# Performance work log

Hardware: AMD Instinct MI355X
Metric: run time of the kernel (lower is better)

## Reference

```python
import jax, jax.numpy as jnp
import numpy as np

B, C, H, W = 16, 512, 32, 32
G = min(C // 4, 32)  # group-norm groups = 32
EPS = 1e-6


def setup_inputs() -> dict:
    key = jax.random.key(0)
    ks = jax.random.split(key, 9)
    s = 1.0 / np.sqrt(C)
    return {
        "x": jax.random.normal(ks[0], (B, C, H, W), dtype=jnp.float32),
        "gn_gamma": jnp.ones((C,), jnp.float32),
        "gn_beta": jnp.zeros((C,), jnp.float32),
        "W0": jax.random.normal(ks[1], (C, C), jnp.float32) * s,
        "b0": jnp.zeros((C,), jnp.float32),
        "W1": jax.random.normal(ks[2], (C, C), jnp.float32) * s,
        "b1": jnp.zeros((C,), jnp.float32),
        "W2": jax.random.normal(ks[3], (C, C), jnp.float32) * s,
        "b2": jnp.zeros((C,), jnp.float32),
        "W3": jax.random.normal(ks[4], (C, C), jnp.float32) * s,
        "b3": jnp.zeros((C,), jnp.float32),
    }


def _group_norm(x, gamma, beta):
    b, c, h, w = x.shape
    xg = x.reshape(b, G, c // G, h, w)
    mu = jnp.mean(xg, axis=(2, 3, 4), keepdims=True)
    var = jnp.var(xg, axis=(2, 3, 4), keepdims=True)
    xn = ((xg - mu) * jax.lax.rsqrt(var + EPS)).reshape(b, c, h, w)
    return xn * gamma[None, :, None, None] + beta[None, :, None, None]


def _nin(x, Wm, bv):
    # 1x1 conv via channel contraction: bchw,cd->bdhw
    return jnp.einsum('bchw,cd->bdhw', x, Wm) + bv[None, :, None, None]


def reference(x, gn_gamma, gn_beta, W0, b0, W1, b1, W2, b2, W3, b3):
    b, c, h, w = x.shape
    hn = _group_norm(x, gn_gamma, gn_beta)
    q = _nin(hn, W0, b0)
    k = _nin(hn, W1, b1)
    v = _nin(hn, W2, b2)
    # attention scores over all spatial positions: [b, h, w, i, j]
    scores = jnp.einsum('bchw,bcij->bhwij', q, k) * (c ** -0.5)
    attn = jax.nn.softmax(scores.reshape(b, h, w, h * w), axis=-1).reshape(b, h, w, h, w)
    o = jnp.einsum('bhwij,bcij->bchw', attn, v)
    o = _nin(o, W3, b3)
    return x + o  # skip_rescale=False
```

## Files before the change

### kernel.cpp

```cpp
#include <hip/hip_runtime.h>
#include <stdint.h>

typedef __bf16 bf16_t;
typedef _Float16 f16_t;
typedef bf16_t bf16x8 __attribute__((ext_vector_type(8)));
typedef bf16_t bf16x4 __attribute__((ext_vector_type(4)));
typedef f16_t  f16x8  __attribute__((ext_vector_type(8)));
typedef float floatx4 __attribute__((ext_vector_type(4)));

static constexpr int NB  = 16;
static constexpr int NC  = 512;
static constexpr int NHW = 1024;
static constexpr int NG  = 32;
static constexpr int CPG = 16;

#define SCALE 0.044194173824159216f
#define LOG2E 1.4426950408889634f

__global__ __launch_bounds__(256) void gn_stats_k(const float* __restrict__ x,
                                                  float* __restrict__ stats) {
  int bg = blockIdx.x;
  const float* xp = x + (size_t)bg * CPG * NHW;
  float s = 0.f, ss = 0.f;
  for (int i = threadIdx.x * 4; i < CPG * NHW; i += 256 * 4) {
    float4 v = *(const float4*)&xp[i];
    s += v.x + v.y + v.z + v.w;
    ss += v.x * v.x + v.y * v.y + v.z * v.z + v.w * v.w;
  }
#pragma unroll
  for (int off = 1; off < 64; off <<= 1) {
    s  += __shfl_xor(s,  off, 64);
    ss += __shfl_xor(ss, off, 64);
  }
  __shared__ float red[2][4];
  int wv = threadIdx.x >> 6;
  if ((threadIdx.x & 63) == 0) { red[0][wv] = s; red[1][wv] = ss; }
  __syncthreads();
  if (threadIdx.x == 0) {
    float st  = red[0][0] + red[0][1] + red[0][2] + red[0][3];
    float sst = red[1][0] + red[1][1] + red[1][2] + red[1][3];
    float mean = st * (1.f / 16384.f);
    float var  = sst * (1.f / 16384.f) - mean * mean;
    stats[bg * 2]     = mean;
    stats[bg * 2 + 1] = rsqrtf(var + 1e-6f);
  }
}

__global__ __launch_bounds__(256) void gn_apply_k(const float* __restrict__ x,
                                                  const float* __restrict__ gamma,
                                                  const float* __restrict__ beta,
                                                  const float* __restrict__ stats,
                                                  bf16_t* __restrict__ hnT) {
  int bi = blockIdx.z;
  int c0 = blockIdx.y * 32;
  int n0 = blockIdx.x * 32;
  __shared__ float tile[32][33];
  int tn = threadIdx.x & 31;
  int tr = threadIdx.x >> 5;
  const float* xb = x + (size_t)bi * NC * NHW;
#pragma unroll
  for (int r = 0; r < 4; r++) {
    int c = c0 + tr + r * 8;
    int g = c >> 4;
    float mean = stats[(bi * NG + g) * 2];
    float rstd = stats[(bi * NG + g) * 2 + 1];
    float ga = gamma[c], be = beta[c];
    float v = xb[(size_t)c * NHW + n0 + tn];
    tile[tr + r * 8][tn] = (v - mean) * rstd * ga + be;
  }
  __syncthreads();
  bf16_t* hb = hnT + (size_t)bi * NHW * NC;
#pragma unroll
  for (int r = 0; r < 4; r++)
    hb[(size_t)(n0 + tr + r * 8) * NC + c0 + tn] = (bf16_t)tile[tn][tr + r * 8];
}

__global__ __launch_bounds__(256) void wtrans_k(const float* __restrict__ W0,
                                                const float* __restrict__ W1,
                                                const float* __restrict__ W2,
                                                const float* __restrict__ W3,
                                                bf16_t* __restrict__ Wt) {
  int w = blockIdx.z;
  const float* W = (w == 0) ? W0 : (w == 1) ? W1 : (w == 2) ? W2 : W3;
  int d0 = blockIdx.x * 32, c0 = blockIdx.y * 32;
  __shared__ float tile[32][33];
  int tdx = threadIdx.x & 31, tr = threadIdx.x >> 5;
#pragma unroll
  for (int r = 0; r < 4; r++)
    tile[tr + r * 8][tdx] = W[(size_t)(c0 + tr + r * 8) * NC + d0 + tdx];
  __syncthreads();
  bf16_t* o = Wt + (size_t)w * NC * NC;
#pragma unroll
  for (int r = 0; r < 4; r++)
    o[(size_t)(d0 + tr + r * 8) * NC + c0 + tdx] = (bf16_t)tile[tdx][tr + r * 8];
}

__device__ __forceinline__ void glds16(const bf16_t* g, bf16_t* lds) {
  __builtin_amdgcn_global_load_lds(
      (const __attribute__((address_space(1))) unsigned int*)g,
      (__attribute__((address_space(3))) unsigned int*)lds, 16, 0, 0);
}

template<int KDIM>
__device__ __forceinline__ void gemm_core128(const bf16_t* __restrict__ A,
                                             const bf16_t* __restrict__ B,
                                             int m0, int n0,
                                             floatx4 (&acc)[4][4]) {
  __shared__ bf16_t As[128 * 32];
  __shared__ bf16_t Bs[128 * 32];
  const int tid = threadIdx.x, lane = tid & 63, wv = tid >> 6;
  const int l16 = lane & 15, quad = lane >> 4;
  const int wm = wv & 1, wn = wv >> 1;

  const bf16_t* aptr = A + (size_t)(m0 + wv * 32 + (lane >> 2)) * KDIM + (lane & 3) * 8;
  const bf16_t* bptr = B + (size_t)(n0 + wv * 32 + (lane >> 2)) * KDIM + (lane & 3) * 8;
  bf16_t* as0 = &As[(wv * 32) * 32];
  bf16_t* as1 = &As[(wv * 32 + 16) * 32];
  bf16_t* bs0 = &Bs[(wv * 32) * 32];
  bf16_t* bs1 = &Bs[(wv * 32 + 16) * 32];

  for (int k0 = 0; k0 < KDIM; k0 += 32) {
    __syncthreads();
    glds16(aptr, as0);
    glds16(aptr + (size_t)16 * KDIM, as1);
    glds16(bptr, bs0);
    glds16(bptr + (size_t)16 * KDIM, bs1);
    aptr += 32; bptr += 32;
    __syncthreads();
    bf16x8 af[4], bfv[4];
#pragma unroll
    for (int i = 0; i < 4; i++)
      af[i] = *(const bf16x8*)&As[(wm * 64 + i * 16 + l16) * 32 + quad * 8];
#pragma unroll
    for (int j = 0; j < 4; j++)
      bfv[j] = *(const bf16x8*)&Bs[(wn * 64 + j * 16 + l16) * 32 + quad * 8];
#pragma unroll
    for (int i = 0; i < 4; i++)
#pragma unroll
      for (int j = 0; j < 4; j++)
        acc[i][j] = __builtin_amdgcn_mfma_f32_16x16x32_bf16(af[i], bfv[j], acc[i][j], 0, 0, 0);
  }
}

__global__ __launch_bounds__(256) void gemm_qkv2_k(const bf16_t* __restrict__ hnT,
                                                   const bf16_t* __restrict__ Wt,
                                                   const float* __restrict__ b0,
                                                   const float* __restrict__ b1,
                                                   const float* __restrict__ b2,
                                                   bf16_t* __restrict__ Qt,
                                                   bf16_t* __restrict__ Kt,
                                                   bf16_t* __restrict__ Vm) {
  int bz = blockIdx.z, bi = bz & 15, wsel = bz >> 4;
  int n0 = blockIdx.x * 128, m0 = blockIdx.y * 128;
  const bf16_t* A = hnT + (size_t)bi * NHW * NC;
  const bf16_t* B = Wt + (size_t)wsel * NC * NC;
  floatx4 acc[4][4];
#pragma unroll
  for (int i = 0; i < 4; i++)
#pragma unroll
    for (int j = 0; j < 4; j++) acc[i][j] = (floatx4){0.f, 0.f, 0.f, 0.f};
  gemm_core128<NC>(A, B, m0, n0, acc);

  const int lane = threadIdx.x & 63, wv = threadIdx.x >> 6;
  const int l16 = lane & 15, quad = lane >> 4, wm = wv & 1, wn = wv >> 1;
  const float* bias = (wsel == 0) ? b0 : (wsel == 1) ? b1 : b2;
  if (wsel < 2) {
    bf16_t* out = ((wsel == 0) ? Qt : Kt) + (size_t)bi * NHW * NC;
#pragma unroll
    for (int i = 0; i < 4; i++)
#pragma unroll
      for (int j = 0; j < 4; j++) {
        int row = m0 + wm * 64 + i * 16 + quad * 4;
        int col = n0 + wn * 64 + j * 16 + l16;
        float bv = bias[col];
#pragma unroll
        for (int r = 0; r < 4; r++)
          out[(size_t)(row + r) * NC + col] = (bf16_t)(acc[i][j][r] + bv);
      }
  } else {
    bf16_t* out = Vm + (size_t)bi * NC * NHW;
#pragma unroll
    for (int i = 0; i < 4; i++)
#pragma unroll
      for (int j = 0; j < 4; j++) {
        int row = m0 + wm * 64 + i * 16 + quad * 4;
        int col = n0 + wn * 64 + j * 16 + l16;
        float bv = bias[col];
        bf16x4 pk;
#pragma unroll
        for (int r = 0; r < 4; r++) pk[r] = (bf16_t)(acc[i][j][r] + bv);
        *(bf16x4*)&out[(size_t)col * NHW + row] = pk;
      }
  }
}

__global__ __launch_bounds__(256) void gemm_s_k(const bf16_t* __restrict__ Qt,
                                                const bf16_t* __restrict__ Kt,
                                                f16_t* __restrict__ S) {
  int bi = blockIdx.z;
  int n0 = blockIdx.x * 128, m0 = blockIdx.y * 128;
  const bf16_t* A = Qt + (size_t)bi * NHW * NC;
  const bf16_t* B = Kt + (size_t)bi * NHW * NC;
  floatx4 acc[4][4];
#pragma unroll
  for (int i = 0; i < 4; i++)
#pragma unroll
    for (int j = 0; j < 4; j++) acc[i][j] = (floatx4){0.f, 0.f, 0.f, 0.f};
  gemm_core128<NC>(A, B, m0, n0, acc);

  const int lane = threadIdx.x & 63, wv = threadIdx.x >> 6;
  const int l16 = lane & 15, quad = lane >> 4, wm = wv & 1, wn = wv >> 1;
  f16_t* out = S + (size_t)bi * NHW * NHW;
#pragma unroll
  for (int i = 0; i < 4; i++)
#pragma unroll
    for (int j = 0; j < 4; j++) {
      int row = m0 + wm * 64 + i * 16 + quad * 4;
      int col = n0 + wn * 64 + j * 16 + l16;
#pragma unroll
      for (int r = 0; r < 4; r++)
        out[(size_t)(row + r) * NHW + col] = (f16_t)(acc[i][j][r] * SCALE);
    }
}

__global__ __launch_bounds__(256) void softmax_k(const f16_t* __restrict__ S,
                                                 bf16_t* __restrict__ P) {
  int row = blockIdx.x * 4 + (threadIdx.x >> 6);
  int lane = threadIdx.x & 63;
  const f16_t* sp = S + (size_t)row * NHW + lane * 16;
  f16x8 a = *(const f16x8*)sp;
  f16x8 b = *(const f16x8*)(sp + 8);
  float v[16];
#pragma unroll
  for (int k = 0; k < 8; k++) { v[k] = (float)a[k]; v[8 + k] = (float)b[k]; }
  float mx = v[0];
#pragma unroll
  for (int k = 1; k < 16; k++) mx = fmaxf(mx, v[k]);
#pragma unroll
  for (int off = 1; off < 64; off <<= 1) mx = fmaxf(mx, __shfl_xor(mx, off, 64));
  float e[16], s = 0.f;
#pragma unroll
  for (int k = 0; k < 16; k++) { e[k] = exp2f((v[k] - mx) * LOG2E); s += e[k]; }
#pragma unroll
  for (int off = 1; off < 64; off <<= 1) s += __shfl_xor(s, off, 64);
  float inv = 1.f / s;
  bf16x8 o0, o1;
#pragma unroll
  for (int k = 0; k < 8; k++) { o0[k] = (bf16_t)(e[k] * inv); o1[k] = (bf16_t)(e[8 + k] * inv); }
  bf16_t* pp = P + (size_t)row * NHW + lane * 16;
  *(bf16x8*)pp = o0;
  *(bf16x8*)(pp + 8) = o1;
}

__global__ __launch_bounds__(256) void gemm_pv_k(const bf16_t* __restrict__ P,
                                                 const bf16_t* __restrict__ Vm,
                                                 bf16_t* __restrict__ Ot) {
  int bi = blockIdx.z;
  int n0 = blockIdx.x * 128, m0 = blockIdx.y * 128;
  const bf16_t* A = P + (size_t)bi * NHW * NHW;
  const bf16_t* B = Vm + (size_t)bi * NC * NHW;
  floatx4 acc[4][4];
#pragma unroll
  for (int i = 0; i < 4; i++)
#pragma unroll
    for (int j = 0; j < 4; j++) acc[i][j] = (floatx4){0.f, 0.f, 0.f, 0.f};
  gemm_core128<NHW>(A, B, m0, n0, acc);

  const int lane = threadIdx.x & 63, wv = threadIdx.x >> 6;
  const int l16 = lane & 15, quad = lane >> 4, wm = wv & 1, wn = wv >> 1;
  bf16_t* out = Ot + (size_t)bi * NHW * NC;
#pragma unroll
  for (int i = 0; i < 4; i++)
#pragma unroll
    for (int j = 0; j < 4; j++) {
      int row = m0 + wm * 64 + i * 16 + quad * 4;
      int col = n0 + wn * 64 + j * 16 + l16;
#pragma unroll
      for (int r = 0; r < 4; r++)
        out[(size_t)(row + r) * NC + col] = (bf16_t)(acc[i][j][r]);
    }
}

__global__ __launch_bounds__(256) void gemm_fin_k(const bf16_t* __restrict__ Ot,
                                                  const bf16_t* __restrict__ W3t,
                                                  const float* __restrict__ b3,
                                                  const float* __restrict__ x,
                                                  float* __restrict__ outp) {
  int bi = blockIdx.z;
  int n0 = blockIdx.x * 128, m0 = blockIdx.y * 128;
  const bf16_t* A = Ot + (size_t)bi * NHW * NC;
  floatx4 acc[4][4];
#pragma unroll
  for (int i = 0; i < 4; i++)
#pragma unroll
    for (int j = 0; j < 4; j++) acc[i][j] = (floatx4){0.f, 0.f, 0.f, 0.f};
  gemm_core128<NC>(A, W3t, m0, n0, acc);

  const int lane = threadIdx.x & 63, wv = threadIdx.x >> 6;
  const int l16 = lane & 15, quad = lane >> 4, wm = wv & 1, wn = wv >> 1;
  const float* xb = x + (size_t)bi * NC * NHW;
  float* ob = outp + (size_t)bi * NC * NHW;
#pragma unroll
  for (int i = 0; i < 4; i++)
#pragma unroll
    for (int j = 0; j < 4; j++) {
      int row = m0 + wm * 64 + i * 16 + quad * 4;
      int col = n0 + wn * 64 + j * 16 + l16;
      float bv = b3[col];
      size_t base = (size_t)col * NHW + row;
      float4 xv = *(const float4*)&xb[base];
      float4 pk;
      pk.x = acc[i][j][0] + bv + xv.x;
      pk.y = acc[i][j][1] + bv + xv.y;
      pk.z = acc[i][j][2] + bv + xv.z;
      pk.w = acc[i][j][3] + bv + xv.w;
      *(float4*)&ob[base] = pk;
    }
}

extern "C" void kernel_launch(void* const* d_in, const int* in_sizes, int n_in,
                              void* d_out, int out_size, void* d_ws, size_t ws_size,
                              hipStream_t stream) {
  (void)in_sizes; (void)n_in; (void)out_size; (void)ws_size;
  const float* x     = (const float*)d_in[0];
  const float* gamma = (const float*)d_in[1];
  const float* beta  = (const float*)d_in[2];
  const float* W0    = (const float*)d_in[3];
  const float* b0    = (const float*)d_in[4];
  const float* W1    = (const float*)d_in[5];
  const float* b1    = (const float*)d_in[6];
  const float* W2    = (const float*)d_in[7];
  const float* b2    = (const float*)d_in[8];
  const float* W3    = (const float*)d_in[9];
  const float* b3    = (const float*)d_in[10];
  float* outp = (float*)d_out;

  char* ws = (char*)d_ws;
  const size_t PLANE = (size_t)NB * NHW * NC * sizeof(bf16_t);
  float* stats = (float*)ws;
  size_t off = 4096;
  bf16_t* hnT = (bf16_t*)(ws + off); off += PLANE;
  bf16_t* Qt  = (bf16_t*)(ws + off); off += PLANE;
  bf16_t* Kt  = (bf16_t*)(ws + off); off += PLANE;
  bf16_t* Vm  = (bf16_t*)(ws + off); off += PLANE;
  bf16_t* Wt  = (bf16_t*)(ws + off); off += 4 * (size_t)NC * NC * sizeof(bf16_t);
  f16_t*  S   = (f16_t*)(ws + off);  off += (size_t)NB * NHW * NHW * sizeof(f16_t);
  bf16_t* P   = (bf16_t*)S;
  bf16_t* Ot  = hnT;

  gn_stats_k<<<NB * NG, 256, 0, stream>>>(x, stats);
  gn_apply_k<<<dim3(32, 16, NB), 256, 0, stream>>>(x, gamma, beta, stats, hnT);
  wtrans_k<<<dim3(16, 16, 4), 256, 0, stream>>>(W0, W1, W2, W3, Wt);
  gemm_qkv2_k<<<dim3(4, 8, 48), 256, 0, stream>>>(hnT, Wt, b0, b1, b2, Qt, Kt, Vm);
  gemm_s_k<<<dim3(8, 8, NB), 256, 0, stream>>>(Qt, Kt, S);
  softmax_k<<<dim3(NB * NHW / 4), 256, 0, stream>>>(S, P);
  gemm_pv_k<<<dim3(4, 8, NB), 256, 0, stream>>>(P, Vm, Ot);
  gemm_fin_k<<<dim3(4, 8, NB), 256, 0, stream>>>(Ot, Wt + 3 * (size_t)NC * NC, b3, x, outp);
}
```

Before: 259.6 us.

## Widen GEMM K-tile to 64 with XOR-swizzled LDS and vectorized epilogue stores

The shared GEMM core now stages 64-wide K tiles, with an XOR swizzle on the LDS chunk index to avoid bank conflicts. This halves the number of barrier pairs per K loop. A SWAP template option exchanges the MFMA operands so that row-major outputs (Q/K, S, PV) can be written as packed 4-element vector stores instead of scattered scalar stores. The QKV GEMM is split into separate Q/K and V kernels, and the transpose kernels now write packed bf16x4. The cost is double the LDS per block, which may lower occupancy.

```diff
diff --git a/kernel.cpp b/kernel.cpp
--- a/kernel.cpp
+++ b/kernel.cpp
@@ -6,6 +6,7 @@
 typedef bf16_t bf16x8 __attribute__((ext_vector_type(8)));
 typedef bf16_t bf16x4 __attribute__((ext_vector_type(4)));
 typedef f16_t  f16x8  __attribute__((ext_vector_type(8)));
+typedef f16_t  f16x4  __attribute__((ext_vector_type(4)));
 typedef float floatx4 __attribute__((ext_vector_type(4)));
 
 static constexpr int NB  = 16;
@@ -70,9 +71,11 @@
   }
   __syncthreads();
   bf16_t* hb = hnT + (size_t)bi * NHW * NC;
-#pragma unroll
-  for (int r = 0; r < 4; r++)
-    hb[(size_t)(n0 + tr + r * 8) * NC + c0 + tn] = (bf16_t)tile[tn][tr + r * 8];
+  int nl = threadIdx.x >> 3, cc = (threadIdx.x & 7) * 4;
+  bf16x4 pk;
+#pragma unroll
+  for (int i = 0; i < 4; i++) pk[i] = (bf16_t)tile[cc + i][nl];
+  *(bf16x4*)&hb[(size_t)(n0 + nl) * NC + c0 + cc] = pk;
 }
 
 __global__ __launch_bounds__(256) void wtrans_k(const float* __restrict__ W0,
@@ -90,9 +93,11 @@
     tile[tr + r * 8][tdx] = W[(size_t)(c0 + tr + r * 8) * NC + d0 + tdx];
   __syncthreads();
   bf16_t* o = Wt + (size_t)w * NC * NC;
-#pragma unroll
-  for (int r = 0; r < 4; r++)
-    o[(size_t)(d0 + tr + r * 8) * NC + c0 + tdx] = (bf16_t)tile[tdx][tr + r * 8];
+  int dl = threadIdx.x >> 3, cc = (threadIdx.x & 7) * 4;
+  bf16x4 pk;
+#pragma unroll
+  for (int i = 0; i < 4; i++) pk[i] = (bf16_t)tile[cc + i][dl];
+  *(bf16x4*)&o[(size_t)(d0 + dl) * NC + c0 + cc] = pk;
 }
 
 __device__ __forceinline__ void glds16(const bf16_t* g, bf16_t* lds) {
@@ -101,97 +106,123 @@
       (__attribute__((address_space(3))) unsigned int*)lds, 16, 0, 0);
 }
 
-template<int KDIM>
-__device__ __forceinline__ void gemm_core128(const bf16_t* __restrict__ A,
-                                             const bf16_t* __restrict__ B,
-                                             int m0, int n0,
-                                             floatx4 (&acc)[4][4]) {
-  __shared__ bf16_t As[128 * 32];
-  __shared__ bf16_t Bs[128 * 32];
+__device__ __forceinline__ floatx4 mfma_bf16(bf16x8 a, bf16x8 b, floatx4 c) {
+  return __builtin_amdgcn_mfma_f32_16x16x32_bf16(a, b, c, 0, 0, 0);
+}
+
+template<int KDIM, bool SWAP>
+__device__ __forceinline__ void gemm_core(const bf16_t* __restrict__ A,
+                                          const bf16_t* __restrict__ B,
+                                          int m0, int n0,
+                                          floatx4 (&acc)[4][4]) {
+  __shared__ bf16_t As[128 * 64];
+  __shared__ bf16_t Bs[128 * 64];
   const int tid = threadIdx.x, lane = tid & 63, wv = tid >> 6;
   const int l16 = lane & 15, quad = lane >> 4;
   const int wm = wv & 1, wn = wv >> 1;
-
-  const bf16_t* aptr = A + (size_t)(m0 + wv * 32 + (lane >> 2)) * KDIM + (lane & 3) * 8;
-  const bf16_t* bptr = B + (size_t)(n0 + wv * 32 + (lane >> 2)) * KDIM + (lane & 3) * 8;
-  bf16_t* as0 = &As[(wv * 32) * 32];
-  bf16_t* as1 = &As[(wv * 32 + 16) * 32];
-  bf16_t* bs0 = &Bs[(wv * 32) * 32];
-  bf16_t* bs1 = &Bs[(wv * 32 + 16) * 32];
-
-  for (int k0 = 0; k0 < KDIM; k0 += 32) {
+  const int x7 = l16 & 7;
+
+  const int srow = lane >> 3;
+  const int schunk = (lane & 7) ^ srow;
+  const bf16_t* aptr = A + (size_t)(m0 + wv * 32 + srow) * KDIM + schunk * 8;
+  const bf16_t* bptr = B + (size_t)(n0 + wv * 32 + srow) * KDIM + schunk * 8;
+  bf16_t* as_ = &As[(wv * 32) * 64];
+  bf16_t* bs_ = &Bs[(wv * 32) * 64];
+
+  for (int k0 = 0; k0 < KDIM; k0 += 64) {
     __syncthreads();
-    glds16(aptr, as0);
-    glds16(aptr + (size_t)16 * KDIM, as1);
-    glds16(bptr, bs0);
-    glds16(bptr + (size_t)16 * KDIM, bs1);
-    aptr += 32; bptr += 32;
+#pragma unroll
+    for (int i = 0; i < 4; i++) {
+      glds16(aptr + (size_t)(8 * i) * KDIM, as_ + (8 * i) * 64);
+      glds16(bptr + (size_t)(8 * i) * KDIM, bs_ + (8 * i) * 64);
+    }
+    aptr += 64; bptr += 64;
     __syncthreads();
-    bf16x8 af[4], bfv[4];
-#pragma unroll
-    for (int i = 0; i < 4; i++)
-      af[i] = *(const bf16x8*)&As[(wm * 64 + i * 16 + l16) * 32 + quad * 8];
-#pragma unroll
-    for (int j = 0; j < 4; j++)
-      bfv[j] = *(const bf16x8*)&Bs[(wn * 64 + j * 16 + l16) * 32 + quad * 8];
-#pragma unroll
-    for (int i = 0; i < 4; i++)
-#pragma unroll
-      for (int j = 0; j < 4; j++)
-        acc[i][j] = __builtin_amdgcn_mfma_f32_16x16x32_bf16(af[i], bfv[j], acc[i][j], 0, 0, 0);
-  }
-}
-
-__global__ __launch_bounds__(256) void gemm_qkv2_k(const bf16_t* __restrict__ hnT,
-                                                   const bf16_t* __restrict__ Wt,
-                                                   const float* __restrict__ b0,
-                                                   const float* __restrict__ b1,
-                                                   const float* __restrict__ b2,
-                                                   bf16_t* __restrict__ Qt,
-                                                   bf16_t* __restrict__ Kt,
-                                                   bf16_t* __restrict__ Vm) {
+    bf16x8 af[2][4], bfv[2][4];
+#pragma unroll
+    for (int h = 0; h < 2; h++)
+#pragma unroll
+      for (int i = 0; i < 4; i++) {
+        int q = h * 4 + quad;
+        af[h][i]  = *(const bf16x8*)&As[(wm * 64 + i * 16 + l16) * 64 + ((q ^ x7) * 8)];
+        bfv[h][i] = *(const bf16x8*)&Bs[(wn * 64 + i * 16 + l16) * 64 + ((q ^ x7) * 8)];
+      }
+#pragma unroll
+    for (int h = 0; h < 2; h++)
+#pragma unroll
+      for (int i = 0; i < 4; i++)
+#pragma unroll
+        for (int j = 0; j < 4; j++)
+          acc[i][j] = SWAP ? mfma_bf16(bfv[h][j], af[h][i], acc[i][j])
+                           : mfma_bf16(af[h][i], bfv[h][j], acc[i][j]);
+  }
+}
+
+#define ACC_INIT(acc)                                   \
+  floatx4 acc[4][4];                                    \
+  _Pragma("unroll") for (int i = 0; i < 4; i++)         \
+  _Pragma("unroll") for (int j = 0; j < 4; j++)         \
+    acc[i][j] = (floatx4){0.f, 0.f, 0.f, 0.f};
+
+__global__ __launch_bounds__(256) void gemm_qk_k(const bf16_t* __restrict__ hnT,
+                                                 const bf16_t* __restrict__ Wt,
+                                                 const float* __restrict__ b0,
+                                                 const float* __restrict__ b1,
+                                                 bf16_t* __restrict__ Qt,
+                                                 bf16_t* __restrict__ Kt) {
   int bz = blockIdx.z, bi = bz & 15, wsel = bz >> 4;
   int n0 = blockIdx.x * 128, m0 = blockIdx.y * 128;
   const bf16_t* A = hnT + (size_t)bi * NHW * NC;
   const bf16_t* B = Wt + (size_t)wsel * NC * NC;
-  floatx4 acc[4][4];
+  ACC_INIT(acc);
+  gemm_core<NC, true>(A, B, m0, n0, acc);
+
+  const int lane = threadIdx.x & 63, wv = threadIdx.x >> 6;
+  const int l16 = lane & 15, quad = lane >> 4, wm = wv & 1, wn = wv >> 1;
+  const float* bias = wsel ? b1 : b0;
+  bf16_t* out = (wsel ? Kt : Qt) + (size_t)bi * NHW * NC;
+#pragma unroll
+  for (int i = 0; i < 4; i++) {
+    int m = m0 + wm * 64 + i * 16 + l16;
+#pragma unroll
+    for (int j = 0; j < 4; j++) {
+      int db = n0 + wn * 64 + j * 16 + quad * 4;
+      float4 bv = *(const float4*)&bias[db];
+      bf16x4 pk;
+      pk[0] = (bf16_t)(acc[i][j][0] + bv.x);
+      pk[1] = (bf16_t)(acc[i][j][1] + bv.y);
+      pk[2] = (bf16_t)(acc[i][j][2] + bv.z);
+      pk[3] = (bf16_t)(acc[i][j][3] + bv.w);
+      *(bf16x4*)&out[(size_t)m * NC + db] = pk;
+    }
+  }
+}
+
+__global__ __launch_bounds__(256) void gemm_v_k(const bf16_t* __restrict__ hnT,
+                                                const bf16_t* __restrict__ Wt2,
+                                                const float* __restrict__ b2,
+                                                bf16_t* __restrict__ Vm) {
+  int bi = blockIdx.z;
+  int n0 = blockIdx.x * 128, m0 = blockIdx.y * 128;
+  const bf16_t* A = hnT + (size_t)bi * NHW * NC;
+  ACC_INIT(acc);
+  gemm_core<NC, false>(A, Wt2, m0, n0, acc);
+
+  const int lane = threadIdx.x & 63, wv = threadIdx.x >> 6;
+  const int l16 = lane & 15, quad = lane >> 4, wm = wv & 1, wn = wv >> 1;
+  bf16_t* out = Vm + (size_t)bi * NC * NHW;
 #pragma unroll
   for (int i = 0; i < 4; i++)
 #pragma unroll
-    for (int j = 0; j < 4; j++) acc[i][j] = (floatx4){0.f, 0.f, 0.f, 0.f};
-  gemm_core128<NC>(A, B, m0, n0, acc);
-
-  const int lane = threadIdx.x & 63, wv = threadIdx.x >> 6;
-  const int l16 = lane & 15, quad = lane >> 4, wm = wv & 1, wn = wv >> 1;
-  const float* bias = (wsel == 0) ? b0 : (wsel == 1) ? b1 : b2;
-  if (wsel < 2) {
-    bf16_t* out = ((wsel == 0) ? Qt : Kt) + (size_t)bi * NHW * NC;
-#pragma unroll
-    for (int i = 0; i < 4; i++)
-#pragma unroll
-      for (int j = 0; j < 4; j++) {
-        int row = m0 + wm * 64 + i * 16 + quad * 4;
-        int col = n0 + wn * 64 + j * 16 + l16;
-        float bv = bias[col];
-#pragma unroll
-        for (int r = 0; r < 4; r++)
-          out[(size_t)(row + r) * NC + col] = (bf16_t)(acc[i][j][r] + bv);
-      }
-  } else {
-    bf16_t* out = Vm + (size_t)bi * NC * NHW;
-#pragma unroll
-    for (int i = 0; i < 4; i++)
-#pragma unroll
-      for (int j = 0; j < 4; j++) {
-        int row = m0 + wm * 64 + i * 16 + quad * 4;
-        int col = n0 + wn * 64 + j * 16 + l16;
-        float bv = bias[col];
-        bf16x4 pk;
-#pragma unroll
-        for (int r = 0; r < 4; r++) pk[r] = (bf16_t)(acc[i][j][r] + bv);
-        *(bf16x4*)&out[(size_t)col * NHW + row] = pk;
-      }
-  }
+    for (int j = 0; j < 4; j++) {
+      int row = m0 + wm * 64 + i * 16 + quad * 4;
+      int col = n0 + wn * 64 + j * 16 + l16;
+      float bv = b2[col];
+      bf16x4 pk;
+#pragma unroll
+      for (int r = 0; r < 4; r++) pk[r] = (bf16_t)(acc[i][j][r] + bv);
+      *(bf16x4*)&out[(size_t)col * NHW + row] = pk;
+    }
 }
 
 __global__ __launch_bounds__(256) void gemm_s_k(const bf16_t* __restrict__ Qt,
@@ -201,26 +232,24 @@
   int n0 = blockIdx.x * 128, m0 = blockIdx.y * 128;
   const bf16_t* A = Qt + (size_t)bi * NHW * NC;
   const bf16_t* B = Kt + (size_t)bi * NHW * NC;
-  floatx4 acc[4][4];
-#pragma unroll
-  for (int i = 0; i < 4; i++)
-#pragma unroll
-    for (int j = 0; j < 4; j++) acc[i][j] = (floatx4){0.f, 0.f, 0.f, 0.f};
-  gemm_core128<NC>(A, B, m0, n0, acc);
+  ACC_INIT(acc);
+  gemm_core<NC, true>(A, B, m0, n0, acc);
 
   const int lane = threadIdx.x & 63, wv = threadIdx.x >> 6;
   const int l16 = lane & 15, quad = lane >> 4, wm = wv & 1, wn = wv >> 1;
   f16_t* out = S + (size_t)bi * NHW * NHW;
 #pragma unroll
-  for (int i = 0; i < 4; i++)
-#pragma unroll
-    for (int j = 0; j < 4; j++) {
-      int row = m0 + wm * 64 + i * 16 + quad * 4;
-      int col = n0 + wn * 64 + j * 16 + l16;
-#pragma unroll
-      for (int r = 0; r < 4; r++)
-        out[(size_t)(row + r) * NHW + col] = (f16_t)(acc[i][j][r] * SCALE);
-    }
+  for (int i = 0; i < 4; i++) {
+    int m = m0 + wm * 64 + i * 16 + l16;
+#pragma unroll
+    for (int j = 0; j < 4; j++) {
+      int nb = n0 + wn * 64 + j * 16 + quad * 4;
+      f16x4 pk;
+#pragma unroll
+      for (int r = 0; r < 4; r++) pk[r] = (f16_t)(acc[i][j][r] * SCALE);
+      *(f16x4*)&out[(size_t)m * NHW + nb] = pk;
+    }
+  }
 }
 
 __global__ __launch_bounds__(256) void softmax_k(const f16_t* __restrict__ S,
@@ -259,26 +288,24 @@
   int n0 = blockIdx.x * 128, m0 = blockIdx.y * 128;
   const bf16_t* A = P + (size_t)bi * NHW * NHW;
   const bf16_t* B = Vm + (size_t)bi * NC * NHW;
-  floatx4 acc[4][4];
-#pragma unroll
-  for (int i = 0; i < 4; i++)
-#pragma unroll
-    for (int j = 0; j < 4; j++) acc[i][j] = (floatx4){0.f, 0.f, 0.f, 0.f};
-  gemm_core128<NHW>(A, B, m0, n0, acc);
+  ACC_INIT(acc);
+  gemm_core<NHW, true>(A, B, m0, n0, acc);
 
   const int lane = threadIdx.x & 63, wv = threadIdx.x >> 6;
   const int l16 = lane & 15, quad = lane >> 4, wm = wv & 1, wn = wv >> 1;
   bf16_t* out = Ot + (size_t)bi * NHW * NC;
 #pragma unroll
-  for (int i = 0; i < 4; i++)
-#pragma unroll
-    for (int j = 0; j < 4; j++) {
-      int row = m0 + wm * 64 + i * 16 + quad * 4;
-      int col = n0 + wn * 64 + j * 16 + l16;
-#pragma unroll
-      for (int r = 0; r < 4; r++)
-        out[(size_t)(row + r) * NC + col] = (bf16_t)(acc[i][j][r]);
-    }
+  for (int i = 0; i < 4; i++) {
+    int m = m0 + wm * 64 + i * 16 + l16;
+#pragma unroll
+    for (int j = 0; j < 4; j++) {
+      int cb = n0 + wn * 64 + j * 16 + quad * 4;
+      bf16x4 pk;
+#pragma unroll
+      for (int r = 0; r < 4; r++) pk[r] = (bf16_t)(acc[i][j][r]);
+      *(bf16x4*)&out[(size_t)m * NC + cb] = pk;
+    }
+  }
 }
 
 __global__ __launch_bounds__(256) void gemm_fin_k(const bf16_t* __restrict__ Ot,
@@ -289,12 +316,8 @@
   int bi = blockIdx.z;
   int n0 = blockIdx.x * 128, m0 = blockIdx.y * 128;
   const bf16_t* A = Ot + (size_t)bi * NHW * NC;
-  floatx4 acc[4][4];
-#pragma unroll
-  for (int i = 0; i < 4; i++)
-#pragma unroll
-    for (int j = 0; j < 4; j++) acc[i][j] = (floatx4){0.f, 0.f, 0.f, 0.f};
-  gemm_core128<NC>(A, W3t, m0, n0, acc);
+  ACC_INIT(acc);
+  gemm_core<NC, false>(A, W3t, m0, n0, acc);
 
   const int lane = threadIdx.x & 63, wv = threadIdx.x >> 6;
   const int l16 = lane & 15, quad = lane >> 4, wm = wv & 1, wn = wv >> 1;
@@ -351,7 +374,8 @@
   gn_stats_k<<<NB * NG, 256, 0, stream>>>(x, stats);
   gn_apply_k<<<dim3(32, 16, NB), 256, 0, stream>>>(x, gamma, beta, stats, hnT);
   wtrans_k<<<dim3(16, 16, 4), 256, 0, stream>>>(W0, W1, W2, W3, Wt);
-  gemm_qkv2_k<<<dim3(4, 8, 48), 256, 0, stream>>>(hnT, Wt, b0, b1, b2, Qt, Kt, Vm);
+  gemm_qk_k<<<dim3(4, 8, 32), 256, 0, stream>>>(hnT, Wt, b0, b1, Qt, Kt);
+  gemm_v_k<<<dim3(4, 8, NB), 256, 0, stream>>>(hnT, Wt + 2 * (size_t)NC * NC, b2, Vm);
   gemm_s_k<<<dim3(8, 8, NB), 256, 0, stream>>>(Qt, Kt, S);
   softmax_k<<<dim3(NB * NHW / 4), 256, 0, stream>>>(S, P);
   gemm_pv_k<<<dim3(4, 8, NB), 256, 0, stream>>>(P, Vm, Ot);
```

After: 257.9 us. No clear change (-0.7%).
